# Optimization experiments

Measured on AMD Instinct MI355X. Metric: run time of the kernel, lower is better.

Reference implementation:

```python
import jax, jax.numpy as jnp
import numpy as np

B, T, C = 4, 1024, 768
H, HS = 12, 64           # num_heads, head_size
VD = 2 * HS              # value dim per head


def setup_inputs() -> dict:
    key = jax.random.key(0)
    ks = jax.random.split(key, 16)
    s = 0.02
    inp = {
        "x": jax.random.normal(ks[0], (B, T, C), jnp.float32),
        "Wq1": jax.random.normal(ks[1], (H, C, HS), jnp.float32) * s,
        "Wk1": jax.random.normal(ks[2], (H, C, HS), jnp.float32) * s,
        "Wq2": jax.random.normal(ks[3], (H, C, HS), jnp.float32) * s,
        "Wk2": jax.random.normal(ks[4], (H, C, HS), jnp.float32) * s,
        "Wv": jax.random.normal(ks[5], (H, C, VD), jnp.float32) * s,
        "lq1": jax.random.normal(ks[6], (H, HS), jnp.float32) * 0.1,
        "lk1": jax.random.normal(ks[7], (H, HS), jnp.float32) * 0.1,
        "lq2": jax.random.normal(ks[8], (H, HS), jnp.float32) * 0.1,
        "lk2": jax.random.normal(ks[9], (H, HS), jnp.float32) * 0.1,
        "gn_w": jnp.ones((H * VD,), jnp.float32),
        "gn_b": jnp.zeros((H * VD,), jnp.float32),
        "Wp": jax.random.normal(ks[10], (C, H * VD), jnp.float32) * s,
        "bp": jnp.zeros((C,), jnp.float32),
        "layer_idx": 3,
    }
    return inp


def _diff_attn(x, Wq1, Wk1, Wq2, Wk2, Wv, lq1, lk1, lq2, lk2,
               gn_w, gn_b, Wp, bp, layer_idx):
    Bc, Tc, _ = x.shape
    scale = 1.0 / jnp.sqrt(jnp.float32(HS))
    # per-head projections: [B,H,T,HS]
    q1 = jnp.einsum('btc,hcd->bhtd', x, Wq1)
    k1 = jnp.einsum('btc,hcd->bhtd', x, Wk1)
    q2 = jnp.einsum('btc,hcd->bhtd', x, Wq2)
    k2 = jnp.einsum('btc,hcd->bhtd', x, Wk2)
    v = jnp.einsum('btc,hce->bhte', x, Wv)           # [B,H,T,2HS]
    mask = jnp.tril(jnp.ones((Tc, Tc), bool))         # causal
    neg = jnp.float32(-jnp.inf)
    a1 = jnp.einsum('bhtd,bhsd->bhts', q1, k1) * scale
    a2 = jnp.einsum('bhtd,bhsd->bhts', q2, k2) * scale
    a1 = jax.nn.softmax(jnp.where(mask, a1, neg), axis=-1)
    a2 = jax.nn.softmax(jnp.where(mask, a2, neg), axis=-1)
    # dynamic lambda init, per get_lambda
    li = jnp.float32(layer_idx)
    dyn = 0.8 - 0.6 * jnp.exp(-0.3 * (li - 1.0))
    lam = jnp.mean(jnp.exp(lq1 * lk1) - jnp.exp(lq2 * lk2) + dyn, axis=-1)  # [H]
    diff = a1 - lam[None, :, None, None] * a2
    out = jnp.einsum('bhts,bhse->bhte', diff, v)      # [B,H,T,2HS]
    out = out.transpose(0, 2, 1, 3).reshape(Bc, Tc, H * VD)
    # GroupLayerNorm == full layernorm over last dim (unbiased=False var)
    mu = out.mean(-1, keepdims=True)
    var = jnp.mean((out - mu) ** 2, axis=-1, keepdims=True)
    out = (out - mu) / jnp.sqrt(var + 1e-5) * gn_w + gn_b
    out = out * 0.2  # (1 - lambda_init_buffer=0.8), buffer never updated
    return out @ Wp.T + bp


def reference(x, Wq1, Wk1, Wq2, Wk2, Wv, lq1, lk1, lq2, lk2,
              gn_w, gn_b, Wp, bp, layer_idx):
    return _diff_attn(x, Wq1, Wk1, Wq2, Wk2, Wv, lq1, lk1, lq2, lk2,
                      gn_w, gn_b, Wp, bp, layer_idx)
```

## Files before the change

kernel.cpp:

```cpp
#include <hip/hip_runtime.h>
#include <hip/hip_bf16.h>

#define Bc   4
#define Tc   1024
#define Cc   768
#define Hc   12
#define HSc  64
#define VDc  128
#define NQKV 4608
#define YLD  3072
#define NROWS 4096
#define HVD  1536

#define Q1OFF 0
#define K1OFF 768
#define Q2OFF 1536
#define K2OFF 2304

typedef __bf16 bf16x8 __attribute__((ext_vector_type(8)));
typedef float f32x4 __attribute__((ext_vector_type(4)));
typedef unsigned int u32x4 __attribute__((ext_vector_type(4)));

#define EXP2SCALE 0.18033688011112042f

static __device__ __forceinline__ float bf2f(unsigned short s) {
    return __uint_as_float(((unsigned int)s) << 16);
}
static __device__ __forceinline__ unsigned short f2bf(float f) {
    unsigned int u = __float_as_uint(f);
    unsigned int r = (u + 0x7FFFu + ((u >> 16) & 1u)) >> 16;
    return (unsigned short)r;
}
static __device__ __forceinline__ unsigned int pack2bf(float lo, float hi) {
    unsigned int a = (__float_as_uint(lo) + 0x8000u) >> 16;
    unsigned int b = (__float_as_uint(hi) + 0x8000u) & 0xFFFF0000u;
    return a | b;
}
static __device__ __forceinline__ float fast_exp2(float x) {
    float r;
    asm("v_exp_f32 %0, %1" : "=v"(r) : "v"(x));
    return r;
}

static __device__ __forceinline__ void load16_lds(const void* g, void* l) {
    __builtin_amdgcn_global_load_lds(
        (const __attribute__((address_space(1))) void*)g,
        (__attribute__((address_space(3))) void*)l, 16, 0, 0);
}

__global__ __launch_bounds__(256) void prep(
    const float* __restrict__ x, const float* __restrict__ Wp,
    const float* __restrict__ lq1, const float* __restrict__ lk1,
    const float* __restrict__ lq2, const float* __restrict__ lk2,
    const int* __restrict__ layer_idx,
    unsigned short* __restrict__ Xb, unsigned short* __restrict__ Wpb,
    float* __restrict__ lam)
{
    int bid = blockIdx.x, tid = threadIdx.x;
    if (bid < 3072) {
        size_t i = (size_t)bid * 256 + tid;
        float4 v = *(const float4*)(x + i * 4);
        ushort4 u;
        u.x = f2bf(v.x); u.y = f2bf(v.y); u.z = f2bf(v.z); u.w = f2bf(v.w);
        *(ushort4*)(Xb + i * 4) = u;
    } else if (bid < 4224) {
        size_t i = (size_t)(bid - 3072) * 256 + tid;
        float4 v = *(const float4*)(Wp + i * 4);
        ushort4 u;
        u.x = f2bf(v.x); u.y = f2bf(v.y); u.z = f2bf(v.z); u.w = f2bf(v.w);
        *(ushort4*)(Wpb + i * 4) = u;
    } else if (tid < 64) {
        int h = bid - 4224, l = tid;
        float li = (float)layer_idx[0];
        float dyn = 0.8f - 0.6f * expf(-0.3f * (li - 1.0f));
        int i = h * HSc + l;
        float v = expf(lq1[i] * lk1[i]) - expf(lq2[i] * lk2[i]) + dyn;
        #pragma unroll
        for (int off = 32; off; off >>= 1) v += __shfl_xor(v, off);
        if (l == 0) lam[h] = v * (1.0f / 64.0f);
    }
}

__global__ __launch_bounds__(256) void trans_w(
    const float* __restrict__ Wq1, const float* __restrict__ Wk1,
    const float* __restrict__ Wq2, const float* __restrict__ Wk2,
    const float* __restrict__ Wv, unsigned short* __restrict__ WcatT)
{
    __shared__ float tile[64][65];
    int tid = threadIdx.x;
    int t = blockIdx.x;
    int kt = t % 12, nt = t / 12;
    int k0 = kt * 64, n0 = nt * 64;
    const float* src;
    int stride;
    if (n0 < 3072) {
        int which = n0 / 768, m = n0 - which * 768, h = m >> 6;
        const float* W = (which == 0) ? Wq1 : (which == 1) ? Wk1 : (which == 2) ? Wq2 : Wk2;
        src = W + ((size_t)h * 768 + k0) * 64;
        stride = 64;
    } else {
        int rel = n0 - 3072, h = rel >> 7, e0 = rel & 127;
        src = Wv + ((size_t)h * 768 + k0) * 128 + e0;
        stride = 128;
    }
    for (int i = tid; i < 4096; i += 256) {
        int kl = i >> 6, dl = i & 63;
        tile[dl][kl] = src[(size_t)kl * stride + dl];
    }
    __syncthreads();
    for (int i = tid; i < 4096; i += 256) {
        int nl = i >> 6, kl = i & 63;
        WcatT[(size_t)(n0 + nl) * 768 + k0 + kl] = f2bf(tile[nl][kl]);
    }
}

template<int TN, int KD, int LDC, bool OUT_BIAS, bool SPLITV>
__global__ __launch_bounds__(256) void gemm_mfma(
    const unsigned short* __restrict__ A, const unsigned short* __restrict__ Bt,
    unsigned short* __restrict__ Cb, float* __restrict__ Cf,
    const float* __restrict__ bias, unsigned short* __restrict__ VtOut)
{
    constexpr int BN = TN * 32;
    constexpr int JB = TN / 2;
    __shared__ unsigned short As[128 * 64];
    __shared__ unsigned short Bs[BN * 64];
    int tid = threadIdx.x, lane = tid & 63, w = tid >> 6;
    int wm = w >> 1, wn = w & 1;

    int bid = blockIdx.x;
    int xcd = bid & 7;
    int idx = bid >> 3;
    int mi  = idx & 3;
    int ni  = idx >> 2;
    int m0 = (xcd * 4 + mi) * 128;
    int n0 = ni * BN;

    int lr = lane >> 2, lq = lane & 3;
    const unsigned short* gA[2];
    const unsigned short* gB[JB];
    #pragma unroll
    for (int j = 0; j < 2; ++j) {
        int row = w * 32 + j * 16 + lr;
        int qg = lq ^ ((row >> 1) & 3);
        gA[j] = A + (size_t)(m0 + row) * KD + qg * 8;
    }
    #pragma unroll
    for (int j = 0; j < JB; ++j) {
        int row = w * (JB * 16) + j * 16 + lr;
        int qg = lq ^ ((row >> 1) & 3);
        gB[j] = Bt + (size_t)(n0 + row) * KD + qg * 8;
    }

    int rr = lane & 15, qd = lane >> 4;
    const unsigned short* aAddr[4];
    const unsigned short* bAddr[TN];
    #pragma unroll
    for (int i = 0; i < 4; ++i) {
        int row = wm * 64 + i * 16 + rr;
        int qs = qd ^ ((row >> 1) & 3);
        aAddr[i] = As + row * 32 + qs * 8;
    }
    #pragma unroll
    for (int t = 0; t < TN; ++t) {
        int row = wn * (TN * 16) + t * 16 + rr;
        int qs = qd ^ ((row >> 1) & 3);
        bAddr[t] = Bs + row * 32 + qs * 8;
    }

    f32x4 acc[4][TN];
    #pragma unroll
    for (int i = 0; i < 4; ++i)
        #pragma unroll
        for (int t = 0; t < TN; ++t) acc[i][t] = {0.f, 0.f, 0.f, 0.f};

    for (int k = 0; k < KD / 64; ++k) {
        __syncthreads();
        load16_lds(gA[0], As + (w * 2 + 0) * 512);
        load16_lds(gA[1], As + (w * 2 + 1) * 512);
        load16_lds(gA[0] + 32, As + 4096 + (w * 2 + 0) * 512);
        load16_lds(gA[1] + 32, As + 4096 + (w * 2 + 1) * 512);
        #pragma unroll
        for (int j = 0; j < JB; ++j) {
            load16_lds(gB[j], Bs + (w * JB + j) * 512);
            load16_lds(gB[j] + 32, Bs + BN * 32 + (w * JB + j) * 512);
        }
        gA[0] += 64; gA[1] += 64;
        #pragma unroll
        for (int j = 0; j < JB; ++j) gB[j] += 64;
        __syncthreads();

        bf16x8 af0[4], af1[4], bf0[TN], bf1[TN];
        #pragma unroll
        for (int i = 0; i < 4; ++i) {
            af0[i] = *(const bf16x8*)aAddr[i];
            af1[i] = *(const bf16x8*)(aAddr[i] + 4096);
        }
        #pragma unroll
        for (int t = 0; t < TN; ++t) {
            bf0[t] = *(const bf16x8*)bAddr[t];
            bf1[t] = *(const bf16x8*)(bAddr[t] + BN * 32);
        }
        #pragma unroll
        for (int i = 0; i < 4; ++i)
            #pragma unroll
            for (int t = 0; t < TN; ++t) {
                acc[i][t] = __builtin_amdgcn_mfma_f32_16x16x32_bf16(af0[i], bf0[t], acc[i][t], 0, 0, 0);
                acc[i][t] = __builtin_amdgcn_mfma_f32_16x16x32_bf16(af1[i], bf1[t], acc[i][t], 0, 0, 0);
            }
    }

    #pragma unroll
    for (int t = 0; t < TN; ++t) {
        int col = n0 + wn * (TN * 16) + t * 16 + rr;
        if (SPLITV && col >= 3072) {
            int rel = col - 3072, hh = rel >> 7, e = rel & 127;
            #pragma unroll
            for (int i = 0; i < 4; ++i) {
                int row0 = m0 + wm * 64 + i * 16 + qd * 4;
                int b = row0 >> 10, tt = row0 & 1023;
                ushort4 pk;
                pk.x = f2bf(acc[i][t][0]); pk.y = f2bf(acc[i][t][1]);
                pk.z = f2bf(acc[i][t][2]); pk.w = f2bf(acc[i][t][3]);
                *(ushort4*)&VtOut[(size_t)((b * Hc + hh) * 128 + e) * 1024 + tt] = pk;
            }
        } else {
            float bv = OUT_BIAS ? bias[col] : 0.f;
            #pragma unroll
            for (int i = 0; i < 4; ++i) {
                #pragma unroll
                for (int r = 0; r < 4; ++r) {
                    int row = m0 + wm * 64 + i * 16 + qd * 4 + r;
                    if (OUT_BIAS)
                        Cf[(size_t)row * LDC + col] = acc[i][t][r] + bv;
                    else
                        Cb[(size_t)row * LDC + col] = f2bf(acc[i][t][r]);
                }
            }
        }
    }
}

__global__ __launch_bounds__(256) void diff_attn_mfma(
    const unsigned short* __restrict__ Y, const unsigned short* __restrict__ Vt,
    const float* __restrict__ lam_buf, unsigned short* __restrict__ attn)
{
    __shared__ __align__(16) unsigned short KVring[2 * 16384];

    int bh = blockIdx.x;
    int b = bh / Hc, h = bh - b * Hc;
    int g = 15 - (int)blockIdx.y;
    int tid = threadIdx.x, lane = tid & 63, wv = tid >> 6;
    int cl = lane & 15, qd = lane >> 4;
    float lamv = lam_buf[h];
    size_t rowbase = (size_t)(b * Tc) * YLD;
    const int hq = h * HSc;
    const unsigned short* VtB = Vt + ((size_t)bh << 17);
    const f32x4 zero4 = {0.f, 0.f, 0.f, 0.f};

    int sub = wv & 1;
    int off8[8];
    int dstoff;
    if (wv < 2) {
        int ksrow = lane >> 3;
        int ksch  = (lane & 7) ^ ksrow;
        #pragma unroll
        for (int j = 0; j < 8; ++j) {
            int moff = (j < 4) ? K1OFF : K2OFF;
            off8[j] = ((j & 3) * 8 + ksrow) * YLD + moff + hq + ksch * 8;
        }
        dstoff = 0;
    } else {
        int vsel = lane >> 2;
        int vsch = (lane & 3) ^ ((vsel >> 1) & 3);
        #pragma unroll
        for (int s = 0; s < 8; ++s)
            off8[s] = (s * 16 + vsel) * 1024 + vsch * 8;
        dstoff = 8192;
    }

    auto stage = [&](int i, int slot) {
        int kt = 2 * i + sub;
        char* base = (char*)KVring + slot * 32768 + sub * 16384 + dstoff;
        const unsigned short* g0 = (wv < 2)
            ? (Y + rowbase + (size_t)(kt * 32) * YLD)
            : (VtB + kt * 32);
        #pragma unroll
        for (int j = 0; j < 8; ++j)
            load16_lds(g0 + off8[j], base + j * 1024);
    };

    int kfo[2][4], vfo[8];
    #pragma unroll
    for (int c = 0; c < 2; ++c) {
        int row = c * 16 + cl;
        #pragma unroll
        for (int j = 0; j < 4; ++j)
            kfo[c][j] = (j >> 1) * 4096 + row * 128 +
                        ((((j & 1) * 4 + qd) ^ (row & 7)) << 4);
    }
    #pragma unroll
    for (int ec = 0; ec < 8; ++ec) {
        int e = ec * 16 + cl;
        vfo[ec] = 8192 + e * 64 + ((qd ^ ((e >> 1) & 3)) << 4);
    }

    int idxA = ((32 * (qd & 1)) + cl) * 4;
    int idxB = idxA + 64;
    bool loHalf = (qd < 2);

    int qrow = g * 64 + wv * 16;

    stage(0, 0);

    size_t qoff = rowbase + (size_t)(qrow + cl) * YLD;
    bf16x8 q1a = *(const bf16x8*)(Y + qoff + Q1OFF + hq + qd * 8);
    bf16x8 q1b = *(const bf16x8*)(Y + qoff + Q1OFF + hq + 32 + qd * 8);
    bf16x8 q2a = *(const bf16x8*)(Y + qoff + Q2OFF + hq + qd * 8);
    bf16x8 q2b = *(const bf16x8*)(Y + qoff + Q2OFF + hq + 32 + qd * 8);

    f32x4 O1[8], O2[8];
    #pragma unroll
    for (int ec = 0; ec < 8; ++ec) { O1[ec] = zero4; O2[ec] = zero4; }
    float l1s = 0.f, l2s = 0.f;

    auto transform = [&](f32x4 S1[2], f32x4 S2[2], int kt,
                         bf16x8& pa1o, bf16x8& pa2o) {
        if (kt * 32 + 31 > qrow) {
            #pragma unroll
            for (int c = 0; c < 2; ++c) {
                int lim = qrow + cl - kt * 32 - c * 16 - qd * 4;
                #pragma unroll
                for (int r = 0; r < 4; ++r) {
                    if (r > lim) { S1[c][r] = -1e30f; S2[c][r] = -1e30f; }
                }
            }
        }
        float p1v[2][4], p2v[2][4];
        #pragma unroll
        for (int c = 0; c < 2; ++c) {
            #pragma unroll
            for (int r = 0; r < 4; ++r) {
                p1v[c][r] = fast_exp2(S1[c][r] * EXP2SCALE);
                p2v[c][r] = fast_exp2(S2[c][r] * EXP2SCALE);
                l1s += p1v[c][r];
                l2s += p2v[c][r];
            }
        }
        unsigned int s1m[2][2], s2m[2][2];
        #pragma unroll
        for (int c = 0; c < 2; ++c) {
            s1m[c][0] = pack2bf(p1v[c][0], p1v[c][1]);
            s1m[c][1] = pack2bf(p1v[c][2], p1v[c][3]);
            s2m[c][0] = pack2bf(p2v[c][0], p2v[c][1]);
            s2m[c][1] = pack2bf(p2v[c][2], p2v[c][3]);
        }
        u32x4 U1, U2;
        {
            int a00 = __builtin_amdgcn_ds_bpermute(idxA, (int)s1m[0][0]);
            int a10 = __builtin_amdgcn_ds_bpermute(idxA, (int)s1m[1][0]);
            int a01 = __builtin_amdgcn_ds_bpermute(idxA, (int)s1m[0][1]);
            int a11 = __builtin_amdgcn_ds_bpermute(idxA, (int)s1m[1][1]);
            int b00 = __builtin_amdgcn_ds_bpermute(idxB, (int)s1m[0][0]);
            int b10 = __builtin_amdgcn_ds_bpermute(idxB, (int)s1m[1][0]);
            int b01 = __builtin_amdgcn_ds_bpermute(idxB, (int)s1m[0][1]);
            int b11 = __builtin_amdgcn_ds_bpermute(idxB, (int)s1m[1][1]);
            U1[0] = (unsigned)(loHalf ? a00 : a10);
            U1[1] = (unsigned)(loHalf ? a01 : a11);
            U1[2] = (unsigned)(loHalf ? b00 : b10);
            U1[3] = (unsigned)(loHalf ? b01 : b11);
        }
        {
            int a00 = __builtin_amdgcn_ds_bpermute(idxA, (int)s2m[0][0]);
            int a10 = __builtin_amdgcn_ds_bpermute(idxA, (int)s2m[1][0]);
            int a01 = __builtin_amdgcn_ds_bpermute(idxA, (int)s2m[0][1]);
            int a11 = __builtin_amdgcn_ds_bpermute(idxA, (int)s2m[1][1]);
            int b00 = __builtin_amdgcn_ds_bpermute(idxB, (int)s2m[0][0]);
            int b10 = __builtin_amdgcn_ds_bpermute(idxB, (int)s2m[1][0]);
            int b01 = __builtin_amdgcn_ds_bpermute(idxB, (int)s2m[0][1]);
            int b11 = __builtin_amdgcn_ds_bpermute(idxB, (int)s2m[1][1]);
            U2[0] = (unsigned)(loHalf ? a00 : a10);
            U2[1] = (unsigned)(loHalf ? a01 : a11);
            U2[2] = (unsigned)(loHalf ? b00 : b10);
            U2[3] = (unsigned)(loHalf ? b01 : b11);
        }
        pa1o = __builtin_bit_cast(bf16x8, U1);
        pa2o = __builtin_bit_cast(bf16x8, U2);
    };

    int NI = g + 1;
    for (int i = 0; i < NI; ++i) {
        asm volatile("s_waitcnt vmcnt(0)\n\ts_barrier" ::: "memory");
        const char* kbA = (const char*)KVring + (i & 1) * 32768;
        const char* kbB = kbA + 16384;
        if (i + 1 < NI) stage(i + 1, (i + 1) & 1);

        bf16x8 kfA[2][4], kfB[2][4];
        #pragma unroll
        for (int c = 0; c < 2; ++c)
            #pragma unroll
            for (int j = 0; j < 4; ++j) {
                kfA[c][j] = *(const bf16x8*)(kbA + kfo[c][j]);
                kfB[c][j] = *(const bf16x8*)(kbB + kfo[c][j]);
            }
        bf16x8 vfA[8];
        #pragma unroll
        for (int ec = 0; ec < 8; ++ec)
            vfA[ec] = *(const bf16x8*)(kbA + vfo[ec]);

        f32x4 S1A[2], S2A[2], S1B[2], S2B[2];
        #pragma unroll
        for (int c = 0; c < 2; ++c) {
            S1A[c] = zero4; S2A[c] = zero4; S1B[c] = zero4; S2B[c] = zero4;
        }
        #pragma unroll
        for (int c = 0; c < 2; ++c) {
            S1A[c] = __builtin_amdgcn_mfma_f32_16x16x32_bf16(kfA[c][0], q1a, S1A[c], 0, 0, 0);
            S1A[c] = __builtin_amdgcn_mfma_f32_16x16x32_bf16(kfA[c][1], q1b, S1A[c], 0, 0, 0);
            S2A[c] = __builtin_amdgcn_mfma_f32_16x16x32_bf16(kfA[c][2], q2a, S2A[c], 0, 0, 0);
            S2A[c] = __builtin_amdgcn_mfma_f32_16x16x32_bf16(kfA[c][3], q2b, S2A[c], 0, 0, 0);
            S1B[c] = __builtin_amdgcn_mfma_f32_16x16x32_bf16(kfB[c][0], q1a, S1B[c], 0, 0, 0);
            S1B[c] = __builtin_amdgcn_mfma_f32_16x16x32_bf16(kfB[c][1], q1b, S1B[c], 0, 0, 0);
            S2B[c] = __builtin_amdgcn_mfma_f32_16x16x32_bf16(kfB[c][2], q2a, S2B[c], 0, 0, 0);
            S2B[c] = __builtin_amdgcn_mfma_f32_16x16x32_bf16(kfB[c][3], q2b, S2B[c], 0, 0, 0);
        }

        bf16x8 pa1A, pa2A, pa1B, pa2B;
        transform(S1A, S2A, 2 * i, pa1A, pa2A);
        bf16x8 vfB[8];
        #pragma unroll
        for (int ec = 0; ec < 8; ++ec)
            vfB[ec] = *(const bf16x8*)(kbB + vfo[ec]);
        transform(S1B, S2B, 2 * i + 1, pa1B, pa2B);

        #pragma unroll
        for (int ec = 0; ec < 8; ++ec) {
            O1[ec] = __builtin_amdgcn_mfma_f32_16x16x32_bf16(pa1A, vfA[ec], O1[ec], 0, 0, 0);
            O2[ec] = __builtin_amdgcn_mfma_f32_16x16x32_bf16(pa2A, vfA[ec], O2[ec], 0, 0, 0);
        }
        #pragma unroll
        for (int ec = 0; ec < 8; ++ec) {
            O1[ec] = __builtin_amdgcn_mfma_f32_16x16x32_bf16(pa1B, vfB[ec], O1[ec], 0, 0, 0);
            O2[ec] = __builtin_amdgcn_mfma_f32_16x16x32_bf16(pa2B, vfB[ec], O2[ec], 0, 0, 0);
        }
    }

    l1s += __shfl_xor(l1s, 16); l1s += __shfl_xor(l1s, 32);
    l2s += __shfl_xor(l2s, 16); l2s += __shfl_xor(l2s, 32);
    float w1[4], w2[4];
    #pragma unroll
    for (int r = 0; r < 4; ++r) {
        float d1 = __shfl(l1s, qd * 4 + r);
        float d2 = __shfl(l2s, qd * 4 + r);
        w1[r] = 1.0f / d1;
        w2[r] = lamv / d2;
    }
    #pragma unroll
    for (int ec = 0; ec < 8; ++ec) {
        #pragma unroll
        for (int r = 0; r < 4; ++r) {
            size_t row = (size_t)(b * Tc + qrow + qd * 4 + r);
            attn[row * HVD + h * VDc + ec * 16 + cl] =
                f2bf(O1[ec][r] * w1[r] - O2[ec][r] * w2[r]);
        }
    }
}

__global__ __launch_bounds__(128) void ln_inplace(
    unsigned short* __restrict__ attn,
    const float* __restrict__ gnw, const float* __restrict__ gnb)
{
    int row = blockIdx.x, tid = threadIdx.x;
    unsigned short* p = attn + (size_t)row * HVD;
    float v[12];
    float s = 0.f, sq = 0.f;
    #pragma unroll
    for (int j = 0; j < 3; ++j) {
        int g = tid + j * 128;
        ushort4 u = *(const ushort4*)(p + g * 4);
        float x0 = bf2f(u.x), x1 = bf2f(u.y), x2 = bf2f(u.z), x3 = bf2f(u.w);
        v[j * 4 + 0] = x0; v[j * 4 + 1] = x1; v[j * 4 + 2] = x2; v[j * 4 + 3] = x3;
        s += x0 + x1 + x2 + x3;
        sq = fmaf(x0, x0, sq); sq = fmaf(x1, x1, sq);
        sq = fmaf(x2, x2, sq); sq = fmaf(x3, x3, sq);
    }
    #pragma unroll
    for (int off = 32; off; off >>= 1) { s += __shfl_xor(s, off); sq += __shfl_xor(sq, off); }
    __shared__ float ss[2], sqs[2];
    if ((tid & 63) == 0) { ss[tid >> 6] = s; sqs[tid >> 6] = sq; }
    __syncthreads();
    float S = ss[0] + ss[1], Q = sqs[0] + sqs[1];
    float mu = S * (1.0f / HVD);
    float rstd = rsqrtf(Q * (1.0f / HVD) - mu * mu + 1e-5f);
    #pragma unroll
    for (int j = 0; j < 3; ++j) {
        int g = tid + j * 128;
        float4 gw = *(const float4*)(gnw + g * 4);
        float4 gb = *(const float4*)(gnb + g * 4);
        ushort4 o;
        o.x = f2bf(((v[j * 4 + 0] - mu) * rstd * gw.x + gb.x) * 0.2f);
        o.y = f2bf(((v[j * 4 + 1] - mu) * rstd * gw.y + gb.y) * 0.2f);
        o.z = f2bf(((v[j * 4 + 2] - mu) * rstd * gw.z + gb.z) * 0.2f);
        o.w = f2bf(((v[j * 4 + 3] - mu) * rstd * gw.w + gb.w) * 0.2f);
        *(ushort4*)(p + g * 4) = o;
    }
}

extern "C" void kernel_launch(void* const* d_in, const int* in_sizes, int n_in,
                              void* d_out, int out_size, void* d_ws, size_t ws_size,
                              hipStream_t stream)
{
    const float* x   = (const float*)d_in[0];
    const float* Wq1 = (const float*)d_in[1];
    const float* Wk1 = (const float*)d_in[2];
    const float* Wq2 = (const float*)d_in[3];
    const float* Wk2 = (const float*)d_in[4];
    const float* Wv  = (const float*)d_in[5];
    const float* lq1 = (const float*)d_in[6];
    const float* lk1 = (const float*)d_in[7];
    const float* lq2 = (const float*)d_in[8];
    const float* lk2 = (const float*)d_in[9];
    const float* gnw = (const float*)d_in[10];
    const float* gnb = (const float*)d_in[11];
    const float* Wp  = (const float*)d_in[12];
    const float* bp  = (const float*)d_in[13];
    const int*   lidx = (const int*)d_in[14];
    float* out = (float*)d_out;

    char* w = (char*)d_ws;
    unsigned short* WcatT = (unsigned short*)(w);
    unsigned short* Xb    = (unsigned short*)(w + 7077888);
    unsigned short* Y     = (unsigned short*)(w + 13369344);
    unsigned short* VtW   = (unsigned short*)(w + 38535168);
    unsigned short* attn  = (unsigned short*)(w + 51118080);
    unsigned short* Wpb   = (unsigned short*)(w + 63700992);
    float* lam            = (float*)(w + 66060288);

    prep<<<dim3(4236), 256, 0, stream>>>(x, Wp, lq1, lk1, lq2, lk2, lidx,
                                         Xb, Wpb, lam);
    trans_w<<<dim3(72 * 12), 256, 0, stream>>>(Wq1, Wk1, Wq2, Wk2, Wv, WcatT);
    gemm_mfma<4, 768, YLD, false, true><<<dim3(1152), 256, 0, stream>>>(
        Xb, WcatT, Y, nullptr, nullptr, VtW);
    diff_attn_mfma<<<dim3(Bc * Hc, 16), 256, 0, stream>>>(Y, VtW, lam, attn);
    ln_inplace<<<dim3(NROWS), 128, 0, stream>>>(attn, gnw, gnb);
    gemm_mfma<2, HVD, Cc, true, false><<<dim3(384), 256, 0, stream>>>(
        attn, Wpb, nullptr, out, bp, nullptr);
}
```

Before: 235.6 us.

## Double-buffer GEMM LDS staging and split-K the output projection with atomics

The shared GEMM kernel now uses a two-slot LDS ring, so the global-to-LDS loads for the next K tile are issued before the MFMAs on the current tile, leaving one barrier per iteration instead of two. The output projection GEMM is split along K into two halves, doubling its block count to 768 so the GPU is better filled, and each half accumulates into the fp32 output with atomicAdd. The prep kernel gains extra blocks that zero the output buffer first. This adds atomic traffic, a zeroing pass and twice the LDS per block, and makes the fp32 summation order nondeterministic.

```diff
diff --git a/kernel.cpp b/kernel.cpp
--- a/kernel.cpp
+++ b/kernel.cpp
@@ -54,7 +54,7 @@
     const float* __restrict__ lq2, const float* __restrict__ lk2,
     const int* __restrict__ layer_idx,
     unsigned short* __restrict__ Xb, unsigned short* __restrict__ Wpb,
-    float* __restrict__ lam)
+    float* __restrict__ lam, float* __restrict__ outz)
 {
     int bid = blockIdx.x, tid = threadIdx.x;
     if (bid < 3072) {
@@ -69,15 +69,21 @@
         ushort4 u;
         u.x = f2bf(v.x); u.y = f2bf(v.y); u.z = f2bf(v.z); u.w = f2bf(v.w);
         *(ushort4*)(Wpb + i * 4) = u;
-    } else if (tid < 64) {
-        int h = bid - 4224, l = tid;
-        float li = (float)layer_idx[0];
-        float dyn = 0.8f - 0.6f * expf(-0.3f * (li - 1.0f));
-        int i = h * HSc + l;
-        float v = expf(lq1[i] * lk1[i]) - expf(lq2[i] * lk2[i]) + dyn;
-        #pragma unroll
-        for (int off = 32; off; off >>= 1) v += __shfl_xor(v, off);
-        if (l == 0) lam[h] = v * (1.0f / 64.0f);
+    } else if (bid < 4236) {
+        if (tid < 64) {
+            int h = bid - 4224, l = tid;
+            float li = (float)layer_idx[0];
+            float dyn = 0.8f - 0.6f * expf(-0.3f * (li - 1.0f));
+            int i = h * HSc + l;
+            float v = expf(lq1[i] * lk1[i]) - expf(lq2[i] * lk2[i]) + dyn;
+            #pragma unroll
+            for (int off = 32; off; off >>= 1) v += __shfl_xor(v, off);
+            if (l == 0) lam[h] = v * (1.0f / 64.0f);
+        }
+    } else {
+        size_t i = (size_t)(bid - 4236) * 256 + tid;
+        float4 z = {0.f, 0.f, 0.f, 0.f};
+        *(float4*)(outz + i * 4) = z;
     }
 }
 
@@ -114,7 +120,7 @@
     }
 }
 
-template<int TN, int KD, int LDC, bool OUT_BIAS, bool SPLITV>
+template<int TN, int KD, int LDC, bool OUT_BIAS, bool SPLITV, int KSPLIT>
 __global__ __launch_bounds__(256) void gemm_mfma(
     const unsigned short* __restrict__ A, const unsigned short* __restrict__ Bt,
     unsigned short* __restrict__ Cb, float* __restrict__ Cf,
@@ -122,18 +128,23 @@
 {
     constexpr int BN = TN * 32;
     constexpr int JB = TN / 2;
-    __shared__ unsigned short As[128 * 64];
-    __shared__ unsigned short Bs[BN * 64];
+    constexpr int ASLOT = 128 * 64;
+    constexpr int SLOT  = ASLOT + BN * 64;
+    __shared__ unsigned short ring[2 * SLOT];
     int tid = threadIdx.x, lane = tid & 63, w = tid >> 6;
     int wm = w >> 1, wn = w & 1;
 
     int bid = blockIdx.x;
     int xcd = bid & 7;
     int idx = bid >> 3;
+    int ks = 0;
+    if (KSPLIT == 2) { ks = idx & 1; idx >>= 1; }
     int mi  = idx & 3;
     int ni  = idx >> 2;
     int m0 = (xcd * 4 + mi) * 128;
     int n0 = ni * BN;
+    constexpr int KLOC = KD / KSPLIT;
+    const int kBase = ks * KLOC;
 
     int lr = lane >> 2, lq = lane & 3;
     const unsigned short* gA[2];
@@ -142,30 +153,43 @@
     for (int j = 0; j < 2; ++j) {
         int row = w * 32 + j * 16 + lr;
         int qg = lq ^ ((row >> 1) & 3);
-        gA[j] = A + (size_t)(m0 + row) * KD + qg * 8;
+        gA[j] = A + (size_t)(m0 + row) * KD + kBase + qg * 8;
     }
     #pragma unroll
     for (int j = 0; j < JB; ++j) {
         int row = w * (JB * 16) + j * 16 + lr;
         int qg = lq ^ ((row >> 1) & 3);
-        gB[j] = Bt + (size_t)(n0 + row) * KD + qg * 8;
+        gB[j] = Bt + (size_t)(n0 + row) * KD + kBase + qg * 8;
     }
 
     int rr = lane & 15, qd = lane >> 4;
-    const unsigned short* aAddr[4];
-    const unsigned short* bAddr[TN];
+    int aOff[4], bOff[TN];
     #pragma unroll
     for (int i = 0; i < 4; ++i) {
         int row = wm * 64 + i * 16 + rr;
         int qs = qd ^ ((row >> 1) & 3);
-        aAddr[i] = As + row * 32 + qs * 8;
+        aOff[i] = row * 32 + qs * 8;
     }
     #pragma unroll
     for (int t = 0; t < TN; ++t) {
         int row = wn * (TN * 16) + t * 16 + rr;
         int qs = qd ^ ((row >> 1) & 3);
-        bAddr[t] = Bs + row * 32 + qs * 8;
-    }
+        bOff[t] = row * 32 + qs * 8;
+    }
+
+    auto stageG = [&](int k, int slot) {
+        unsigned short* s = ring + slot * SLOT;
+        int k64 = k * 64;
+        load16_lds(gA[0] + k64,      s + (w * 2 + 0) * 512);
+        load16_lds(gA[1] + k64,      s + (w * 2 + 1) * 512);
+        load16_lds(gA[0] + k64 + 32, s + 4096 + (w * 2 + 0) * 512);
+        load16_lds(gA[1] + k64 + 32, s + 4096 + (w * 2 + 1) * 512);
+        #pragma unroll
+        for (int j = 0; j < JB; ++j) {
+            load16_lds(gB[j] + k64,      s + ASLOT + (w * JB + j) * 512);
+            load16_lds(gB[j] + k64 + 32, s + ASLOT + BN * 32 + (w * JB + j) * 512);
+        }
+    };
 
     f32x4 acc[4][TN];
     #pragma unroll
@@ -173,32 +197,23 @@
         #pragma unroll
         for (int t = 0; t < TN; ++t) acc[i][t] = {0.f, 0.f, 0.f, 0.f};
 
-    for (int k = 0; k < KD / 64; ++k) {
-        __syncthreads();
-        load16_lds(gA[0], As + (w * 2 + 0) * 512);
-        load16_lds(gA[1], As + (w * 2 + 1) * 512);
-        load16_lds(gA[0] + 32, As + 4096 + (w * 2 + 0) * 512);
-        load16_lds(gA[1] + 32, As + 4096 + (w * 2 + 1) * 512);
-        #pragma unroll
-        for (int j = 0; j < JB; ++j) {
-            load16_lds(gB[j], Bs + (w * JB + j) * 512);
-            load16_lds(gB[j] + 32, Bs + BN * 32 + (w * JB + j) * 512);
-        }
-        gA[0] += 64; gA[1] += 64;
-        #pragma unroll
-        for (int j = 0; j < JB; ++j) gB[j] += 64;
-        __syncthreads();
+    constexpr int NT = KLOC / 64;
+    stageG(0, 0);
+    for (int k = 0; k < NT; ++k) {
+        asm volatile("s_waitcnt vmcnt(0)\n\ts_barrier" ::: "memory");
+        const unsigned short* s = ring + (k & 1) * SLOT;
+        if (k + 1 < NT) stageG(k + 1, (k + 1) & 1);
 
         bf16x8 af0[4], af1[4], bf0[TN], bf1[TN];
         #pragma unroll
         for (int i = 0; i < 4; ++i) {
-            af0[i] = *(const bf16x8*)aAddr[i];
-            af1[i] = *(const bf16x8*)(aAddr[i] + 4096);
+            af0[i] = *(const bf16x8*)(s + aOff[i]);
+            af1[i] = *(const bf16x8*)(s + 4096 + aOff[i]);
         }
         #pragma unroll
         for (int t = 0; t < TN; ++t) {
-            bf0[t] = *(const bf16x8*)bAddr[t];
-            bf1[t] = *(const bf16x8*)(bAddr[t] + BN * 32);
+            bf0[t] = *(const bf16x8*)(s + ASLOT + bOff[t]);
+            bf1[t] = *(const bf16x8*)(s + ASLOT + BN * 32 + bOff[t]);
         }
         #pragma unroll
         for (int i = 0; i < 4; ++i)
@@ -222,6 +237,16 @@
                 pk.x = f2bf(acc[i][t][0]); pk.y = f2bf(acc[i][t][1]);
                 pk.z = f2bf(acc[i][t][2]); pk.w = f2bf(acc[i][t][3]);
                 *(ushort4*)&VtOut[(size_t)((b * Hc + hh) * 128 + e) * 1024 + tt] = pk;
+            }
+        } else if (KSPLIT == 2) {
+            float bv = (OUT_BIAS && ks == 0) ? bias[col] : 0.f;
+            #pragma unroll
+            for (int i = 0; i < 4; ++i) {
+                #pragma unroll
+                for (int r = 0; r < 4; ++r) {
+                    int row = m0 + wm * 64 + i * 16 + qd * 4 + r;
+                    atomicAdd(&Cf[(size_t)row * LDC + col], acc[i][t][r] + bv);
+                }
             }
         } else {
             float bv = OUT_BIAS ? bias[col] : 0.f;
@@ -535,13 +560,13 @@
     unsigned short* Wpb   = (unsigned short*)(w + 63700992);
     float* lam            = (float*)(w + 66060288);
 
-    prep<<<dim3(4236), 256, 0, stream>>>(x, Wp, lq1, lk1, lq2, lk2, lidx,
-                                         Xb, Wpb, lam);
+    prep<<<dim3(7308), 256, 0, stream>>>(x, Wp, lq1, lk1, lq2, lk2, lidx,
+                                         Xb, Wpb, lam, out);
     trans_w<<<dim3(72 * 12), 256, 0, stream>>>(Wq1, Wk1, Wq2, Wk2, Wv, WcatT);
-    gemm_mfma<4, 768, YLD, false, true><<<dim3(1152), 256, 0, stream>>>(
+    gemm_mfma<4, 768, YLD, false, true, 1><<<dim3(1152), 256, 0, stream>>>(
         Xb, WcatT, Y, nullptr, nullptr, VtW);
     diff_attn_mfma<<<dim3(Bc * Hc, 16), 256, 0, stream>>>(Y, VtW, lam, attn);
     ln_inplace<<<dim3(NROWS), 128, 0, stream>>>(attn, gnw, gnb);
-    gemm_mfma<2, HVD, Cc, true, false><<<dim3(384), 256, 0, stream>>>(
+    gemm_mfma<2, HVD, Cc, true, false, 2><<<dim3(768), 256, 0, stream>>>(
         attn, Wpb, nullptr, out, bp, nullptr);
 }
```

Result: no change. 236.8 us (+0.5%).
